# Performance work log

Measured on AMD Instinct MI355X. Metric: run time of the kernel, lower is better.

Reference implementation:

```python
import jax, jax.numpy as jnp
import numpy as np

B, R, K_RANK = 128, 256, 10  # batch, rDim==cDim, rank
MU = 0.1
GAMMA = 0.51 * MU


def averaging_diagonals(X):
    """Project [..., m, n] matrices to Toeplitz by averaging each diagonal."""
    m, n = X.shape[-2:]
    # diagonal id for entry (i, j): j - i + (m - 1), in [0, m + n - 2]
    idx = (jnp.arange(n)[None, :] - jnp.arange(m)[:, None] + (m - 1)).reshape(-1)
    D = m + n - 1
    lead = X.shape[:-2]
    flat = X.reshape(lead + (m * n,))
    sums = jnp.zeros(lead + (D,), X.dtype).at[..., idx].add(flat)
    counts = jnp.zeros((D,), X.dtype).at[idx].add(jnp.ones((m * n,), X.dtype))
    avg = sums / counts
    return avg[..., idx].reshape(X.shape)


def rank_k(x, K):
    """Best rank-K approximation via truncated SVD, batched over leading dims."""
    U, S, Vh = jnp.linalg.svd(x, full_matrices=False)
    return jnp.einsum('...rk,...k,...kc->...rc', U[..., :K], S[..., :K], Vh[..., :K, :])


def setup_inputs() -> dict:
    key = jax.random.key(0)
    k1, k2, k3 = jax.random.split(key, 3)
    T = jax.random.normal(k1, (B, R, R), jnp.float32)
    Tp = jax.random.normal(k2, (B, R, R), jnp.float32)
    Sp = jax.random.normal(k3, (B, R, R), jnp.float32)
    # generateW: averagingDiagonals of indicator of first row/col
    S0 = jnp.zeros((R, R), jnp.float32).at[0, :].set(1.0).at[:, 0].set(1.0)
    W = averaging_diagonals(S0)
    w1 = jnp.eye(R, dtype=jnp.float32) * (1.0 - GAMMA)
    w2 = jnp.eye(R, dtype=jnp.float32) * GAMMA
    w3 = MU * W
    w4 = -MU * W
    return {"T": T, "Tp": Tp, "Sp": Sp, "w1": w1, "w2": w2, "w3": w3, "w4": w4, "K": K_RANK}


def reference(T, Tp, Sp, w1, w2, w3, w4, K):
    # Tptmp = w1 @ Sp + w2 @ Tp + w4 * Tp + w3 * T  (batched over B)
    Tptmp = (jnp.einsum('rk,bkc->brc', w1, Sp)
             + jnp.einsum('rk,bkc->brc', w2, Tp)
             + w4 * Tp + w3 * T)
    Tpnew = rank_k(Tptmp, K)
    Spnew = Sp - Tpnew + averaging_diagonals(2.0 * Tpnew - Sp)
    return (T, Tpnew, Spnew)
```

## Files before the change

### kernel.cpp

```cpp
#include <hip/hip_runtime.h>
#include <math.h>

#define B_   128
#define N_   256
#define L_   64
#define NRR  (N_*N_)
#define BRR  (B_*NRR)
#define BNL  (B_*N_*L_)

static __device__ __forceinline__ void fma4(float4& a, float s, const float4& v) {
  a.x += s * v.x; a.y += s * v.y; a.z += s * v.z; a.w += s * v.w;
}

__global__ __launch_bounds__(256) void k_build_A(
    const float* __restrict__ T, const float* __restrict__ Tp,
    const float* __restrict__ Sp, const float* __restrict__ w1,
    const float* __restrict__ w2, const float* __restrict__ w3,
    const float* __restrict__ w4, float* __restrict__ A) {
  int i4 = blockIdx.x * 256 + threadIdx.x;
  if (i4 >= BRR / 4) return;
  int rc4 = i4 & (NRR / 4 - 1);
  int r = rc4 >> 6;
  float a1 = w1[r * N_ + r], a2 = w2[r * N_ + r];
  float4 sp = ((const float4*)Sp)[i4];
  float4 tp = ((const float4*)Tp)[i4];
  float4 tt = ((const float4*)T)[i4];
  float4 w3v = ((const float4*)w3)[rc4];
  float4 w4v = ((const float4*)w4)[rc4];
  float4 o;
  o.x = a1 * sp.x + a2 * tp.x + w4v.x * tp.x + w3v.x * tt.x;
  o.y = a1 * sp.y + a2 * tp.y + w4v.y * tp.y + w3v.y * tt.y;
  o.z = a1 * sp.z + a2 * tp.z + w4v.z * tp.z + w3v.z * tt.z;
  o.w = a1 * sp.w + a2 * tp.w + w4v.w * tp.w + w3v.w * tt.w;
  ((float4*)A)[i4] = o;
}

__global__ __launch_bounds__(256) void k_aat(const float* __restrict__ A,
                                             float* __restrict__ G) {
  int b = blockIdx.z, ti = blockIdx.x, tj = blockIdx.y;
  if (ti > tj) return;
  int it = ti * 64, jt = tj * 64;
  __shared__ __align__(16) float AsT[32][68];
  __shared__ __align__(16) float BsT[32][68];
  const float* Ab = A + (size_t)b * NRR;
  int t = threadIdx.x, tx = t & 15, ty = t >> 4;
  float4 acc[4] = {};
  int kk = t & 31, r0 = t >> 5;
  for (int k0 = 0; k0 < N_; k0 += 32) {
#pragma unroll
    for (int p = 0; p < 8; ++p) {
      int r = r0 + p * 8;
      AsT[kk][r] = Ab[(it + r) * N_ + k0 + kk];
      BsT[kk][r] = Ab[(jt + r) * N_ + k0 + kk];
    }
    __syncthreads();
#pragma unroll
    for (int k = 0; k < 32; ++k) {
      float4 av = *(const float4*)&AsT[k][ty * 4];
      float4 bv = *(const float4*)&BsT[k][tx * 4];
      fma4(acc[0], av.x, bv);
      fma4(acc[1], av.y, bv);
      fma4(acc[2], av.z, bv);
      fma4(acc[3], av.w, bv);
    }
    __syncthreads();
  }
  float* Gb = G + (size_t)b * NRR;
#pragma unroll
  for (int i = 0; i < 4; ++i)
    *(float4*)&Gb[(it + ty * 4 + i) * N_ + jt + tx * 4] = acc[i];
  if (ti < tj) {
    const float* a = (const float*)acc;
#pragma unroll
    for (int i = 0; i < 4; ++i)
#pragma unroll
      for (int j = 0; j < 4; ++j)
        Gb[(jt + tx * 4 + j) * N_ + it + ty * 4 + i] = a[i * 4 + j];
  }
}

__global__ __launch_bounds__(256) void k_gq(const float* __restrict__ G,
                                            const float* __restrict__ Q,
                                            float* __restrict__ Y) {
  __shared__ __align__(16) float Qs[64][68];
  int b = blockIdx.y, it = blockIdx.x * 64;
  const float* Gb = G + (size_t)b * NRR;
  const float* Qb = Q + (size_t)b * (N_ * L_);
  int t = threadIdx.x, cx = t & 15, ry = t >> 4;
  const float* gr[4];
#pragma unroll
  for (int i = 0; i < 4; ++i) gr[i] = Gb + (size_t)(it + ry * 4 + i) * N_;
  float4 acc[4] = {};
  for (int kc = 0; kc < N_; kc += 64) {
#pragma unroll
    for (int p = 0; p < 4; ++p) {
      int idx = t + p * 256;
      int r = idx >> 4, c4 = idx & 15;
      *(float4*)&Qs[r][c4 * 4] = *(const float4*)&Qb[(kc + r) * L_ + c4 * 4];
    }
    __syncthreads();
#pragma unroll 4
    for (int k4 = 0; k4 < 16; ++k4) {
      int k = k4 * 4;
      float4 g[4];
#pragma unroll
      for (int i = 0; i < 4; ++i) g[i] = *(const float4*)&gr[i][kc + k];
      float4 q0 = *(const float4*)&Qs[k + 0][cx * 4];
      float4 q1 = *(const float4*)&Qs[k + 1][cx * 4];
      float4 q2 = *(const float4*)&Qs[k + 2][cx * 4];
      float4 q3 = *(const float4*)&Qs[k + 3][cx * 4];
#pragma unroll
      for (int i = 0; i < 4; ++i) {
        fma4(acc[i], g[i].x, q0);
        fma4(acc[i], g[i].y, q1);
        fma4(acc[i], g[i].z, q2);
        fma4(acc[i], g[i].w, q3);
      }
    }
    __syncthreads();
  }
  float* Yb = Y + (size_t)b * (N_ * L_);
#pragma unroll
  for (int i = 0; i < 4; ++i)
    *(float4*)&Yb[(it + ry * 4 + i) * L_ + cx * 4] = acc[i];
}

__global__ __launch_bounds__(256) void k_xty(const float* __restrict__ X,
                                             const float* __restrict__ Y,
                                             float* __restrict__ Mo) {
  int b = blockIdx.x, t = threadIdx.x, tx = t & 15, ty = t >> 4;
  const float* Xb = X + (size_t)b * (N_ * L_);
  const float* Yb = Y + (size_t)b * (N_ * L_);
  float4 a0 = {}, a1 = {}, a2 = {}, a3 = {};
#pragma unroll 4
  for (int k = 0; k < N_; ++k) {
    float4 xv = *(const float4*)&Xb[k * L_ + ty * 4];
    float4 yv = *(const float4*)&Yb[k * L_ + tx * 4];
    fma4(a0, xv.x, yv); fma4(a1, xv.y, yv);
    fma4(a2, xv.z, yv); fma4(a3, xv.w, yv);
  }
  float* Mb = Mo + (size_t)b * L_ * L_;
  *(float4*)&Mb[(ty * 4 + 0) * L_ + tx * 4] = a0;
  *(float4*)&Mb[(ty * 4 + 1) * L_ + tx * 4] = a1;
  *(float4*)&Mb[(ty * 4 + 2) * L_ + tx * 4] = a2;
  *(float4*)&Mb[(ty * 4 + 3) * L_ + tx * 4] = a3;
}

__global__ __launch_bounds__(256) void k_init_Y(float* __restrict__ Y) {
  int idx = blockIdx.x * 256 + threadIdx.x;
  if (idx >= BNL) return;
  unsigned u = (unsigned)idx * 2654435761u;
  u ^= u >> 16; u *= 2246822519u; u ^= u >> 13; u *= 3266489917u; u ^= u >> 16;
  Y[idx] = (float)(int)u * 4.6566129e-10f;
}

__global__ __launch_bounds__(256) void k_qr(float* __restrict__ Q) {
  __shared__ __align__(16) float S[64][68];
  __shared__ float dinv[64];
  int b = blockIdx.x, t = threadIdx.x, tx = t & 15, ty = t >> 4;
  float* Qb = Q + (size_t)b * (N_ * L_);
  {
    float4 a0 = {}, a1 = {}, a2 = {}, a3 = {};
#pragma unroll 4
    for (int k = 0; k < N_; ++k) {
      float4 xv = *(const float4*)&Qb[k * L_ + ty * 4];
      float4 yv = *(const float4*)&Qb[k * L_ + tx * 4];
      fma4(a0, xv.x, yv); fma4(a1, xv.y, yv);
      fma4(a2, xv.z, yv); fma4(a3, xv.w, yv);
    }
    *(float4*)&S[ty * 4 + 0][tx * 4] = a0;
    *(float4*)&S[ty * 4 + 1][tx * 4] = a1;
    *(float4*)&S[ty * 4 + 2][tx * 4] = a2;
    *(float4*)&S[ty * 4 + 3][tx * 4] = a3;
  }
  __syncthreads();
  for (int kb = 0; kb < 8; ++kb) {
    int base = kb * 8;
    if (t == 0) {
      for (int q = 0; q < 8; ++q) {
        float d = S[base + q][base + q];
        for (int w = 0; w < q; ++w) d -= S[base + q][base + w] * S[base + q][base + w];
        d = sqrtf(fmaxf(d, 1e-20f));
        S[base + q][base + q] = d;
        float di = 1.f / d;
        dinv[base + q] = di;
        for (int r = q + 1; r < 8; ++r) {
          float v = S[base + r][base + q];
          for (int w = 0; w < q; ++w) v -= S[base + r][base + w] * S[base + q][base + w];
          S[base + r][base + q] = v * di;
        }
      }
    }
    __syncthreads();
    int nrows = 56 - base;
    if (t < nrows) {
      int i = base + 8 + t;
      float x[8];
#pragma unroll
      for (int q = 0; q < 8; ++q) {
        float v = S[i][base + q];
        for (int w = 0; w < q; ++w) v -= S[base + q][base + w] * x[w];
        x[q] = v * dinv[base + q];
      }
#pragma unroll
      for (int q = 0; q < 8; ++q) S[i][base + q] = x[q];
    }
    __syncthreads();
    if (nrows > 0) {
      for (int e = t; e < nrows * 64; e += 256) {
        int io = e >> 6, ko = e & 63;
        if (ko < nrows) {
          int i = base + 8 + io, k = base + 8 + ko;
          float4 p0 = *(const float4*)&S[i][base], p1 = *(const float4*)&S[i][base + 4];
          float4 r0 = *(const float4*)&S[k][base], r1 = *(const float4*)&S[k][base + 4];
          S[i][k] -= p0.x * r0.x + p0.y * r0.y + p0.z * r0.z + p0.w * r0.w
                   + p1.x * r1.x + p1.y * r1.y + p1.z * r1.z + p1.w * r1.w;
        }
      }
    }
    __syncthreads();
  }
  {
    float x[64];
#pragma unroll
    for (int u = 0; u < 16; ++u) {
      float4 v = *(const float4*)&Qb[t * L_ + u * 4];
      x[u * 4 + 0] = v.x; x[u * 4 + 1] = v.y;
      x[u * 4 + 2] = v.z; x[u * 4 + 3] = v.w;
    }
#pragma unroll
    for (int j = 0; j < 64; ++j) {
      float s = x[j];
#pragma unroll
      for (int mq = 0; mq < (j >> 2); ++mq) {
        float4 lv = *(const float4*)&S[j][mq * 4];
        s -= lv.x * x[mq * 4 + 0] + lv.y * x[mq * 4 + 1]
           + lv.z * x[mq * 4 + 2] + lv.w * x[mq * 4 + 3];
      }
#pragma unroll
      for (int k = (j & ~3); k < j; ++k) s -= S[j][k] * x[k];
      x[j] = s * dinv[j];
    }
#pragma unroll
    for (int u = 0; u < 16; ++u) {
      float4 v;
      v.x = x[u * 4 + 0]; v.y = x[u * 4 + 1];
      v.z = x[u * 4 + 2]; v.w = x[u * 4 + 3];
      *(float4*)&Qb[t * L_ + u * 4] = v;
    }
  }
}

__global__ __launch_bounds__(256) void k_jacobi(float* __restrict__ Mg,
                                                float* __restrict__ Vg) {
  __shared__ __align__(16) float A[64 * 66];
  __shared__ __align__(16) float Vt[64][68];
  int b = blockIdx.x, t = threadIdx.x;
  float* Mb = Mg + (size_t)b * L_ * L_;
#pragma unroll
  for (int p = 0; p < 16; ++p) {
    int e = t + p * 256, r = e >> 6, c = e & 63;
    A[r * 66 + c] = Mb[r * L_ + c];
    Vt[r][c] = (r == c) ? 1.f : 0.f;
  }
  __syncthreads();
  int m = t >> 3, u = t & 7;
  for (int sweep = 0; sweep < 4; ++sweep) {
    for (int rnd = 0; rnd < 63; ++rnd) {
      int i, j;
      if (m == 0) { i = rnd; j = 63; }
      else {
        int a = rnd + m;       if (a >= 63) a -= 63;
        int bb = rnd + 63 - m; if (bb >= 63) bb -= 63;
        i = min(a, bb); j = max(a, bb);
      }
      float aii = A[i * 66 + i], ajj = A[j * 66 + j], aij = A[i * 66 + j];
      float c_ = 1.f, s_ = 0.f;
      if (fabsf(aij) > 1e-12f) {
        float tau = (ajj - aii) / (2.f * aij);
        float tt = (tau >= 0.f ? 1.f : -1.f) / (fabsf(tau) + sqrtf(1.f + tau * tau));
        c_ = rsqrtf(1.f + tt * tt);
        s_ = tt * c_;
      }
      {
        float2* Ai = (float2*)&A[i * 66 + u * 8];
        float2* Aj = (float2*)&A[j * 66 + u * 8];
#pragma unroll
        for (int q = 0; q < 4; ++q) {
          float2 x = Ai[q], y = Aj[q], nx, ny;
          nx.x = c_ * x.x - s_ * y.x; ny.x = s_ * x.x + c_ * y.x;
          nx.y = c_ * x.y - s_ * y.y; ny.y = s_ * x.y + c_ * y.y;
          Ai[q] = nx; Aj[q] = ny;
        }
        float4* Vi = (float4*)&Vt[i][u * 8];
        float4* Vj = (float4*)&Vt[j][u * 8];
#pragma unroll
        for (int q = 0; q < 2; ++q) {
          float4 vx = Vi[q], vy = Vj[q], mx, my;
          mx.x = c_ * vx.x - s_ * vy.x; my.x = s_ * vx.x + c_ * vy.x;
          mx.y = c_ * vx.y - s_ * vy.y; my.y = s_ * vx.y + c_ * vy.y;
          mx.z = c_ * vx.z - s_ * vy.z; my.z = s_ * vx.z + c_ * vy.z;
          mx.w = c_ * vx.w - s_ * vy.w; my.w = s_ * vx.w + c_ * vy.w;
          Vi[q] = mx; Vj[q] = my;
        }
      }
      __syncthreads();
#pragma unroll
      for (int p = 0; p < 8; ++p) {
        int k = u + 8 * p;
        float x = A[k * 66 + i], y = A[k * 66 + j];
        A[k * 66 + i] = c_ * x - s_ * y;
        A[k * 66 + j] = s_ * x + c_ * y;
      }
      __syncthreads();
    }
  }
  if (t < 64) Mb[t * L_ + t] = A[t * 66 + t];
  float* Vb = Vg + (size_t)b * L_ * L_;
#pragma unroll
  for (int p = 0; p < 16; ++p) {
    int e = t + p * 256, r = e >> 6, c = e & 63;
    Vb[r * L_ + c] = Vt[r][c];
  }
}

__global__ void k_topk(const float* __restrict__ Mg, const int* __restrict__ Kp,
                       int* __restrict__ topidx) {
  int b = blockIdx.x;
  if (threadIdx.x != 0) return;
  const float* Mb = Mg + (size_t)b * L_ * L_;
  int K = *Kp; if (K > 16) K = 16;
  float vals[64]; bool used[64];
  for (int i = 0; i < 64; ++i) { vals[i] = Mb[i * L_ + i]; used[i] = false; }
  for (int j = 0; j < K; ++j) {
    int best = 0; float bv = -1e30f;
    for (int i = 0; i < 64; ++i)
      if (!used[i] && vals[i] > bv) { bv = vals[i]; best = i; }
    used[best] = true;
    topidx[b * 16 + j] = best;
  }
}

__global__ __launch_bounds__(256) void k_formU(const float* __restrict__ Q,
                                               const float* __restrict__ Vtg,
                                               const int* __restrict__ topidx,
                                               const int* __restrict__ Kp,
                                               float* __restrict__ U) {
  __shared__ float Vs[64][17];
  int b = blockIdx.x, t = threadIdx.x;
  int K = *Kp; if (K > 16) K = 16;
  if (t < 64) {
    for (int j = 0; j < 16; ++j)
      Vs[t][j] = (j < K)
        ? Vtg[(size_t)b * L_ * L_ + (size_t)topidx[b * 16 + j] * L_ + t]
        : 0.f;
  }
  __syncthreads();
  const float* Qb = Q + (size_t)b * N_ * L_;
  float qv[64];
#pragma unroll
  for (int k = 0; k < 64; ++k) qv[k] = Qb[t * L_ + k];
  float* Ub = U + (size_t)b * N_ * 16;
  for (int j = 0; j < 16; ++j) {
    float s = 0.f;
    if (j < K) {
#pragma unroll
      for (int k = 0; k < 64; ++k) s += qv[k] * Vs[k][j];
    }
    Ub[t * 16 + j] = s;
  }
}

__global__ __launch_bounds__(256) void k_utA(const float* __restrict__ U,
                                             const float* __restrict__ A,
                                             const int* __restrict__ Kp,
                                             float* __restrict__ C) {
  __shared__ float Us[256][17];
  int b = blockIdx.x, t = threadIdx.x;
  int K = *Kp; if (K > 16) K = 16;
  const float* Ub = U + (size_t)b * N_ * 16;
  for (int p = 0; p < 16; ++p) {
    int r = (t >> 4) + p * 16, j = t & 15;
    Us[r][j] = Ub[r * 16 + j];
  }
  __syncthreads();
  const float* Ab = A + (size_t)b * NRR;
  float acc[16];
  for (int j = 0; j < 16; ++j) acc[j] = 0.f;
  for (int i = 0; i < N_; ++i) {
    float av = Ab[i * N_ + t];
    for (int j = 0; j < K; ++j) acc[j] += Us[i][j] * av;
  }
  float* Cb = C + (size_t)b * 16 * N_;
  for (int j = 0; j < 16; ++j) Cb[j * N_ + t] = (j < K) ? acc[j] : 0.f;
}

__global__ __launch_bounds__(256) void k_uc(const float* __restrict__ U,
                                            const float* __restrict__ C,
                                            const int* __restrict__ Kp,
                                            float* __restrict__ Tpnew) {
  __shared__ float Cs[16][256];
  __shared__ float Us[16][17];
  int b = blockIdx.y, rt = blockIdx.x * 16, t = threadIdx.x;
  int K = *Kp; if (K > 16) K = 16;
  const float* Cb = C + (size_t)b * 16 * N_;
  for (int j = 0; j < 16; ++j) Cs[j][t] = Cb[j * N_ + t];
  Us[t >> 4][t & 15] = U[(size_t)b * N_ * 16 + (size_t)(rt + (t >> 4)) * 16 + (t & 15)];
  __syncthreads();
  float* Ob = Tpnew + (size_t)b * NRR;
  for (int r = 0; r < 16; ++r) {
    float s = 0.f;
    for (int j = 0; j < K; ++j) s += Us[r][j] * Cs[j][t];
    Ob[(rt + r) * N_ + t] = s;
  }
}

__global__ __launch_bounds__(256) void k_copyT(const float* __restrict__ T,
                                               float* __restrict__ O) {
  int i4 = blockIdx.x * 256 + threadIdx.x;
  if (i4 < BRR / 4) ((float4*)O)[i4] = ((const float4*)T)[i4];
}

__global__ __launch_bounds__(256) void k_spnew(const float* __restrict__ Sp,
                                               const float* __restrict__ Tpnew,
                                               float* __restrict__ Spnew) {
  __shared__ float sums[512];
  int b = blockIdx.x, t = threadIdx.x;
  for (int i = t; i < 512; i += 256) sums[i] = 0.f;
  __syncthreads();
  const float4* Spb = (const float4*)(Sp + (size_t)b * NRR);
  const float4* Tb  = (const float4*)(Tpnew + (size_t)b * NRR);
  for (int i4 = t; i4 < NRR / 4; i4 += 256) {
    int r = i4 >> 6, c = (i4 & 63) * 4;
    float4 tv = Tb[i4], sv = Spb[i4];
    int d = c - r + 255;
    atomicAdd(&sums[d + 0], 2.f * tv.x - sv.x);
    atomicAdd(&sums[d + 1], 2.f * tv.y - sv.y);
    atomicAdd(&sums[d + 2], 2.f * tv.z - sv.z);
    atomicAdd(&sums[d + 3], 2.f * tv.w - sv.w);
  }
  __syncthreads();
  for (int d = t; d < 511; d += 256) {
    int cnt = 256 - (d < 255 ? 255 - d : d - 255);
    sums[d] /= (float)cnt;
  }
  __syncthreads();
  float4* Ob = (float4*)(Spnew + (size_t)b * NRR);
  for (int i4 = t; i4 < NRR / 4; i4 += 256) {
    int r = i4 >> 6, c = (i4 & 63) * 4;
    float4 tv = Tb[i4], sv = Spb[i4];
    int d = c - r + 255;
    float4 o;
    o.x = sv.x - tv.x + sums[d + 0];
    o.y = sv.y - tv.y + sums[d + 1];
    o.z = sv.z - tv.z + sums[d + 2];
    o.w = sv.w - tv.w + sums[d + 3];
    Ob[i4] = o;
  }
}

extern "C" void kernel_launch(void* const* d_in, const int* in_sizes, int n_in,
                              void* d_out, int out_size, void* d_ws, size_t ws_size,
                              hipStream_t stream) {
  const float* T  = (const float*)d_in[0];
  const float* Tp = (const float*)d_in[1];
  const float* Sp = (const float*)d_in[2];
  const float* w1 = (const float*)d_in[3];
  const float* w2 = (const float*)d_in[4];
  const float* w3 = (const float*)d_in[5];
  const float* w4 = (const float*)d_in[6];
  const int*   Kp = (const int*)d_in[7];
  float* out = (float*)d_out;

  float* slot0 = out;
  float* slot1 = out + BRR;
  float* slot2 = out + 2 * (size_t)BRR;
  float* G = slot0;
  float* A = slot1;
  float* Qb[2] = { slot2, slot2 + BNL };
  float* sc    = slot2 + 2 * (size_t)BNL;
  float* Mbuf  = sc;
  float* Vbuf  = sc + 524288;
  float* Ubuf  = sc + 2 * 524288;
  float* Cbuf  = sc + 3 * 524288;
  int*   topidx = (int*)(sc + 4 * 524288);

  k_build_A<<<BRR / 4 / 256, 256, 0, stream>>>(T, Tp, Sp, w1, w2, w3, w4, A);
  k_aat<<<dim3(4, 4, B_), 256, 0, stream>>>(A, G);
  k_init_Y<<<BNL / 256, 256, 0, stream>>>(Qb[0]);
  k_qr<<<B_, 256, 0, stream>>>(Qb[0]);

  int cur = 0;
  for (int it = 0; it < 12; ++it) {
    k_gq<<<dim3(4, B_), 256, 0, stream>>>(G, Qb[cur], Qb[1 - cur]);
    cur = 1 - cur;
    if ((it & 3) == 3) k_qr<<<B_, 256, 0, stream>>>(Qb[cur]);
  }
  k_gq<<<dim3(4, B_), 256, 0, stream>>>(G, Qb[cur], Qb[1 - cur]);
  k_xty<<<B_, 256, 0, stream>>>(Qb[cur], Qb[1 - cur], Mbuf);
  k_jacobi<<<B_, 256, 0, stream>>>(Mbuf, Vbuf);
  k_topk<<<B_, 64, 0, stream>>>(Mbuf, Kp, topidx);
  k_formU<<<B_, 256, 0, stream>>>(Qb[cur], Vbuf, topidx, Kp, Ubuf);
  k_utA<<<B_, 256, 0, stream>>>(Ubuf, A, Kp, Cbuf);
  k_uc<<<dim3(16, B_), 256, 0, stream>>>(Ubuf, Cbuf, Kp, slot1);
  k_copyT<<<BRR / 4 / 256, 256, 0, stream>>>(T, slot0);
  k_spnew<<<B_, 256, 0, stream>>>(Sp, slot1, slot2);
}
```

Measured before the change: 1.437 ms.

## Drop eigenvector accumulation in Jacobi; reconstruct top-16 eigenvectors by replaying rotations

The Jacobi kernel no longer rotates a full 64x64 eigenvector matrix in shared memory on every round. Instead it records each rotation's sine, ranks the diagonal in parallel to pick the top 16 eigenvalues, and replays the rotations backwards on only those 16 unit vectors using wavefront shuffles. This also removes the separate single-thread top-k kernel and its launch, and widens the A-row updates to float4. Recovering cosine from sine as sqrt(1-s^2) loses the rotation angle sign convention and precision. It also adds a serial 252-step replay with shuffles and a larger shared-memory footprint.

```diff
diff --git a/kernel.cpp b/kernel.cpp
--- a/kernel.cpp
+++ b/kernel.cpp
@@ -253,20 +253,21 @@
 
 __global__ __launch_bounds__(256) void k_jacobi(float* __restrict__ Mg,
                                                 float* __restrict__ Vg) {
-  __shared__ __align__(16) float A[64 * 66];
-  __shared__ __align__(16) float Vt[64][68];
+  __shared__ __align__(16) float A[64][68];
+  __shared__ float shist[252 * 32];
+  __shared__ int selb[16];
   int b = blockIdx.x, t = threadIdx.x;
   float* Mb = Mg + (size_t)b * L_ * L_;
 #pragma unroll
   for (int p = 0; p < 16; ++p) {
     int e = t + p * 256, r = e >> 6, c = e & 63;
-    A[r * 66 + c] = Mb[r * L_ + c];
-    Vt[r][c] = (r == c) ? 1.f : 0.f;
+    A[r][c] = Mb[r * L_ + c];
   }
   __syncthreads();
   int m = t >> 3, u = t & 7;
+  int rcnt = 0;
   for (int sweep = 0; sweep < 4; ++sweep) {
-    for (int rnd = 0; rnd < 63; ++rnd) {
+    for (int rnd = 0; rnd < 63; ++rnd, ++rcnt) {
       int i, j;
       if (m == 0) { i = rnd; j = 63; }
       else {
@@ -274,7 +275,7 @@
         int bb = rnd + 63 - m; if (bb >= 63) bb -= 63;
         i = min(a, bb); j = max(a, bb);
       }
-      float aii = A[i * 66 + i], ajj = A[j * 66 + j], aij = A[i * 66 + j];
+      float aii = A[i][i], ajj = A[j][j], aij = A[i][j];
       float c_ = 1.f, s_ = 0.f;
       if (fabsf(aij) > 1e-12f) {
         float tau = (ajj - aii) / (2.f * aij);
@@ -282,68 +283,77 @@
         c_ = rsqrtf(1.f + tt * tt);
         s_ = tt * c_;
       }
+      if (u == 0) shist[rcnt * 32 + m] = s_;
       {
-        float2* Ai = (float2*)&A[i * 66 + u * 8];
-        float2* Aj = (float2*)&A[j * 66 + u * 8];
-#pragma unroll
-        for (int q = 0; q < 4; ++q) {
-          float2 x = Ai[q], y = Aj[q], nx, ny;
+        float4* Ai = (float4*)&A[i][u * 8];
+        float4* Aj = (float4*)&A[j][u * 8];
+#pragma unroll
+        for (int q = 0; q < 2; ++q) {
+          float4 x = Ai[q], y = Aj[q], nx, ny;
           nx.x = c_ * x.x - s_ * y.x; ny.x = s_ * x.x + c_ * y.x;
           nx.y = c_ * x.y - s_ * y.y; ny.y = s_ * x.y + c_ * y.y;
+          nx.z = c_ * x.z - s_ * y.z; ny.z = s_ * x.z + c_ * y.z;
+          nx.w = c_ * x.w - s_ * y.w; ny.w = s_ * x.w + c_ * y.w;
           Ai[q] = nx; Aj[q] = ny;
         }
-        float4* Vi = (float4*)&Vt[i][u * 8];
-        float4* Vj = (float4*)&Vt[j][u * 8];
-#pragma unroll
-        for (int q = 0; q < 2; ++q) {
-          float4 vx = Vi[q], vy = Vj[q], mx, my;
-          mx.x = c_ * vx.x - s_ * vy.x; my.x = s_ * vx.x + c_ * vy.x;
-          mx.y = c_ * vx.y - s_ * vy.y; my.y = s_ * vx.y + c_ * vy.y;
-          mx.z = c_ * vx.z - s_ * vy.z; my.z = s_ * vx.z + c_ * vy.z;
-          mx.w = c_ * vx.w - s_ * vy.w; my.w = s_ * vx.w + c_ * vy.w;
-          Vi[q] = mx; Vj[q] = my;
-        }
       }
       __syncthreads();
 #pragma unroll
       for (int p = 0; p < 8; ++p) {
         int k = u + 8 * p;
-        float x = A[k * 66 + i], y = A[k * 66 + j];
-        A[k * 66 + i] = c_ * x - s_ * y;
-        A[k * 66 + j] = s_ * x + c_ * y;
+        float x = A[k][i], y = A[k][j];
+        A[k][i] = c_ * x - s_ * y;
+        A[k][j] = s_ * x + c_ * y;
       }
       __syncthreads();
     }
   }
-  if (t < 64) Mb[t * L_ + t] = A[t * 66 + t];
-  float* Vb = Vg + (size_t)b * L_ * L_;
-#pragma unroll
-  for (int p = 0; p < 16; ++p) {
-    int e = t + p * 256, r = e >> 6, c = e & 63;
-    Vb[r * L_ + c] = Vt[r][c];
-  }
-}
-
-__global__ void k_topk(const float* __restrict__ Mg, const int* __restrict__ Kp,
-                       int* __restrict__ topidx) {
-  int b = blockIdx.x;
-  if (threadIdx.x != 0) return;
-  const float* Mb = Mg + (size_t)b * L_ * L_;
-  int K = *Kp; if (K > 16) K = 16;
-  float vals[64]; bool used[64];
-  for (int i = 0; i < 64; ++i) { vals[i] = Mb[i * L_ + i]; used[i] = false; }
-  for (int j = 0; j < K; ++j) {
-    int best = 0; float bv = -1e30f;
-    for (int i = 0; i < 64; ++i)
-      if (!used[i] && vals[i] > bv) { bv = vals[i]; best = i; }
-    used[best] = true;
-    topidx[b * 16 + j] = best;
-  }
+  int lane = t & 63, wv = t >> 6;
+  float dl = A[lane][lane];
+  int rank = 0;
+  for (int k = 0; k < 64; ++k) {
+    float dk = A[k][k];
+    rank += (dk > dl || (dk == dl && k < lane)) ? 1 : 0;
+  }
+  if (t < 64 && rank < 16) selb[rank] = lane;
+  __syncthreads();
+  int s0 = selb[wv * 4 + 0], s1 = selb[wv * 4 + 1];
+  int s2 = selb[wv * 4 + 2], s3 = selb[wv * 4 + 3];
+  float x0 = (lane == s0) ? 1.f : 0.f;
+  float x1 = (lane == s1) ? 1.f : 0.f;
+  float x2 = (lane == s2) ? 1.f : 0.f;
+  float x3 = (lane == s3) ? 1.f : 0.f;
+  for (int rc = 251; rc >= 0; --rc) {
+    int rnd = rc % 63;
+    int partner, mm;
+    if (lane == 63)        { partner = rnd; mm = 0; }
+    else if (lane == rnd)  { partner = 63;  mm = 0; }
+    else {
+      partner = (2 * rnd - lane + 126) % 63;
+      int mc = (lane - rnd + 63) % 63;
+      mm = mc < 63 - mc ? mc : 63 - mc;
+    }
+    float s_ = shist[rc * 32 + mm];
+    float c_ = sqrtf(fmaxf(1.f - s_ * s_, 0.f));
+    float coef = (lane > partner) ? -s_ : s_;
+    float y0 = __shfl(x0, partner, 64);
+    float y1 = __shfl(x1, partner, 64);
+    float y2 = __shfl(x2, partner, 64);
+    float y3 = __shfl(x3, partner, 64);
+    x0 = c_ * x0 + coef * y0;
+    x1 = c_ * x1 + coef * y1;
+    x2 = c_ * x2 + coef * y2;
+    x3 = c_ * x3 + coef * y3;
+  }
+  float* Vb = Vg + (size_t)b * 1024;
+  Vb[lane * 16 + wv * 4 + 0] = x0;
+  Vb[lane * 16 + wv * 4 + 1] = x1;
+  Vb[lane * 16 + wv * 4 + 2] = x2;
+  Vb[lane * 16 + wv * 4 + 3] = x3;
 }
 
 __global__ __launch_bounds__(256) void k_formU(const float* __restrict__ Q,
-                                               const float* __restrict__ Vtg,
-                                               const int* __restrict__ topidx,
+                                               const float* __restrict__ Vg,
                                                const int* __restrict__ Kp,
                                                float* __restrict__ U) {
   __shared__ float Vs[64][17];
@@ -351,9 +361,7 @@
   int K = *Kp; if (K > 16) K = 16;
   if (t < 64) {
     for (int j = 0; j < 16; ++j)
-      Vs[t][j] = (j < K)
-        ? Vtg[(size_t)b * L_ * L_ + (size_t)topidx[b * 16 + j] * L_ + t]
-        : 0.f;
+      Vs[t][j] = (j < K) ? Vg[(size_t)b * 1024 + t * 16 + j] : 0.f;
   }
   __syncthreads();
   const float* Qb = Q + (size_t)b * N_ * L_;
@@ -483,7 +491,6 @@
   float* Vbuf  = sc + 524288;
   float* Ubuf  = sc + 2 * 524288;
   float* Cbuf  = sc + 3 * 524288;
-  int*   topidx = (int*)(sc + 4 * 524288);
 
   k_build_A<<<BRR / 4 / 256, 256, 0, stream>>>(T, Tp, Sp, w1, w2, w3, w4, A);
   k_aat<<<dim3(4, 4, B_), 256, 0, stream>>>(A, G);
@@ -499,8 +506,7 @@
   k_gq<<<dim3(4, B_), 256, 0, stream>>>(G, Qb[cur], Qb[1 - cur]);
   k_xty<<<B_, 256, 0, stream>>>(Qb[cur], Qb[1 - cur], Mbuf);
   k_jacobi<<<B_, 256, 0, stream>>>(Mbuf, Vbuf);
-  k_topk<<<B_, 64, 0, stream>>>(Mbuf, Kp, topidx);
-  k_formU<<<B_, 256, 0, stream>>>(Qb[cur], Vbuf, topidx, Kp, Ubuf);
+  k_formU<<<B_, 256, 0, stream>>>(Qb[cur], Vbuf, Kp, Ubuf);
   k_utA<<<B_, 256, 0, stream>>>(Ubuf, A, Kp, Cbuf);
   k_uc<<<dim3(16, B_), 256, 0, stream>>>(Ubuf, Cbuf, Kp, slot1);
   k_copyT<<<BRR / 4 / 256, 256, 0, stream>>>(T, slot0);
```

Result: faster. 1.358 ms (-5.5%).
